# Kernel optimization log

Hardware: AMD Instinct MI355X
Metric: run time of the kernel (lower is better)

The kernel has to match this reference:

```python
import jax, jax.numpy as jnp
import numpy as np

NPOINT = 1024
RADIUS = 0.5
NSAMPLE = 32
BN_EPS = 1e-5


def square_distance(src, dst):
    # src: (B,S,3), dst: (B,N,3) -> (B,S,N)
    return (jnp.sum(src ** 2, -1, keepdims=True)
            + jnp.swapaxes(jnp.sum(dst ** 2, -1, keepdims=True), -2, -1)
            - 2.0 * jnp.einsum('bsc,bnc->bsn', src, dst))


def farthest_point_sample(xyz, npoint):
    # xyz: (B,N,3) -> (B,npoint) int32. Deterministic start at index 0.
    B, N, _ = xyz.shape

    def step(carry, _):
        distance, farthest = carry
        centroid = jnp.take_along_axis(xyz, farthest[:, None, None], axis=1)  # (B,1,3)
        d = jnp.sum((xyz - centroid) ** 2, axis=-1)                           # (B,N)
        distance = jnp.minimum(distance, d)
        nxt = jnp.argmax(distance, axis=-1).astype(jnp.int32)
        return (distance, nxt), farthest

    init = (jnp.full((B, N), 1e10, dtype=xyz.dtype), jnp.zeros((B,), jnp.int32))
    _, cents = jax.lax.scan(step, init, None, length=npoint)  # (npoint,B)
    return cents.T


def ball_query(radius, nsample, xyz, new_xyz):
    # -> (B,S,nsample) int32 indices into N; empty slots padded with first hit.
    B, N, _ = xyz.shape
    dist = square_distance(new_xyz, xyz)                       # (B,S,N)
    base = jnp.arange(N, dtype=jnp.int32)[None, None, :]
    idx = jnp.where(dist <= radius ** 2, base, N)
    idx = jnp.sort(idx, axis=-1)[:, :, :nsample]
    first = idx[:, :, :1]
    return jnp.where(idx == N, first, idx)


def index_points(points, idx):
    # points: (B,N,C), idx: (B,...) -> (B,...,C)
    return jax.vmap(lambda p, i: p[i])(points, idx)


def _forward(xyz, features, params):
    # indices are data-dependent but non-differentiable selections
    xyz_c = jax.lax.stop_gradient(xyz)
    fps_idx = farthest_point_sample(xyz_c, NPOINT)             # (B,S)
    group_idx = ball_query(RADIUS, NSAMPLE, xyz_c, index_points(xyz_c, fps_idx))

    new_xyz = index_points(xyz, fps_idx)                       # (B,S,3)
    grouped_xyz = index_points(xyz, group_idx) - new_xyz[:, :, None, :]  # (B,S,K,3)
    grouped = jnp.concatenate([grouped_xyz, index_points(features, group_idx)], -1)  # (B,S,K,Cin)

    for (w, b, g, be) in params:
        # 1x1 Conv2d == per-point linear; BatchNorm2d in training mode:
        # stats over all but channel axis (here axes 0,1,2 of (B,S,K,C)).
        h = jnp.einsum('bskc,dc->bskd', grouped, w) + b
        mean = jnp.mean(h, axis=(0, 1, 2))
        var = jnp.var(h, axis=(0, 1, 2))
        h = (h - mean) * jax.lax.rsqrt(var + BN_EPS) * g + be
        grouped = jax.nn.gelu(h, approximate=False)

    new_features = jnp.max(grouped, axis=2)                    # (B,S,D)
    return new_xyz, new_features


def setup_inputs() -> dict:
    key = jax.random.key(0)
    ks = jax.random.split(key, 16)
    B, N, C = 16, 4096, 64
    inp = {
        'xyz': jax.random.normal(ks[0], (B, N, 3), jnp.float32),
        'features': jax.random.normal(ks[1], (B, N, C), jnp.float32),
    }
    chans = [67, 64, 64, 128]
    for i in range(3):
        cin, cout = chans[i], chans[i + 1]
        inp[f'w{i}'] = jax.random.normal(ks[2 + 4 * i], (cout, cin), jnp.float32) * (1.0 / np.sqrt(cin))
        inp[f'b{i}'] = jnp.zeros((cout,), jnp.float32)
        inp[f'g{i}'] = jnp.ones((cout,), jnp.float32)
        inp[f'be{i}'] = jnp.zeros((cout,), jnp.float32)
    return inp


def reference(xyz, features, w0, b0, g0, be0, w1, b1, g1, be1, w2, b2, g2, be2):
    params = [(w0, b0, g0, be0), (w1, b1, g1, be1), (w2, b2, g2, be2)]
    return _forward(xyz, features, params)
```

## Files before the change

### kernel.cpp

```cpp
#include <hip/hip_runtime.h>

typedef unsigned int uint;
typedef unsigned short ushort;
typedef unsigned long long ull;

#define NB 16
#define NN 4096
#define NS 1024
#define NK 32
#define CIN0 67
#define NPTS (NB*NS*NK)
#define BN_EPS 1e-5f
#define INV_NPTS (1.0f/524288.0f)

#define W0T_OFF 0
#define W1T_OFF 4288
#define W2T_OFF 8384
#define WT_TOTAL 16576

#define FPS_T 256
#define PPT (NN / FPS_T)

#define KMAX_STEP(K, CTRL) do { \
    uint _lo = (uint)(K), _hi = (uint)((K) >> 32); \
    uint _nlo = (uint)__builtin_amdgcn_update_dpp(0, (int)_lo, (CTRL), 0xF, 0xF, true); \
    uint _nhi = (uint)__builtin_amdgcn_update_dpp(0, (int)_hi, (CTRL), 0xF, 0xF, true); \
    ull _nk = ((ull)_nhi << 32) | _nlo; \
    if (_nk > (K)) (K) = _nk; \
  } while (0)

__device__ __forceinline__ void fps_block_merge(
    const uint2* sk, const float4* sc,
    float& cx, float& cy, float& cz, int& fi)
{
  uint4 e01 = *(const uint4*)&sk[0];
  uint4 e23 = *(const uint4*)&sk[2];
  ull k0 = ((ull)e01.y << 32) | e01.x;
  ull k1 = ((ull)e01.w << 32) | e01.z;
  ull k2 = ((ull)e23.y << 32) | e23.x;
  ull k3 = ((ull)e23.w << 32) | e23.z;
  float4 c0 = sc[0], c1 = sc[1], c2 = sc[2], c3 = sc[3];
  ull b = k0; float4 C = c0;
  if (k1 > b) { b = k1; C = c1; }
  if (k2 > b) { b = k2; C = c2; }
  if (k3 > b) { b = k3; C = c3; }
  cx = C.x; cy = C.y; cz = C.z;
  fi = (int)(~(uint)b);
}

__global__ __launch_bounds__(FPS_T) void fps_kernel(
    const float* __restrict__ xyz, float* __restrict__ centers,
    float* __restrict__ out_newxyz)
{
#pragma clang fp contract(off)
  __shared__ float4 sxyz[NN];
  __shared__ int sfar[NS];
  __shared__ __align__(16) uint2  sk[2][FPS_T/64];
  __shared__ __align__(16) float4 sc[2][FPS_T/64];
  const int b = blockIdx.x;
  const int tid = threadIdx.x;
  const int lane = tid & 63;
  const int wv = tid >> 6;
  const float* xb = xyz + (size_t)b * NN * 3;
  for (int i = tid; i < NN; i += FPS_T)
    sxyz[i] = make_float4(xb[i*3+0], xb[i*3+1], xb[i*3+2], 0.f);
  __syncthreads();
  float px[PPT], py[PPT], pz[PPT], dist[PPT];
  const int base = tid * PPT;
#pragma unroll
  for (int j = 0; j < PPT; ++j) {
    float4 P = sxyz[base+j];
    px[j] = P.x; py[j] = P.y; pz[j] = P.z;
    dist[j] = 1e10f;
  }
  float4 C0 = sxyz[0];
  float cx = C0.x, cy = C0.y, cz = C0.z;
  if (tid == 0) sfar[0] = 0;

  for (int it = 1; it < NS; ++it) {
#pragma unroll
    for (int j = 0; j < PPT; ++j) {
      float dx = px[j]-cx, dy = py[j]-cy, dz = pz[j]-cz;
      float d = (dx*dx + dy*dy) + dz*dz;
      float dd = dist[j];
      dist[j] = d < dd ? d : dd;
    }
    float v8[8]; int i8[8];
#pragma unroll
    for (int j = 0; j < 8; ++j) {
      bool t = dist[2*j+1] > dist[2*j];
      v8[j] = t ? dist[2*j+1] : dist[2*j];
      i8[j] = base + (t ? 2*j+1 : 2*j);
    }
    float v4[4]; int i4[4];
#pragma unroll
    for (int j = 0; j < 4; ++j) {
      bool t = v8[2*j+1] > v8[2*j];
      v4[j] = t ? v8[2*j+1] : v8[2*j];
      i4[j] = t ? i8[2*j+1] : i8[2*j];
    }
    float v2[2]; int i2[2];
#pragma unroll
    for (int j = 0; j < 2; ++j) {
      bool t = v4[2*j+1] > v4[2*j];
      v2[j] = t ? v4[2*j+1] : v4[2*j];
      i2[j] = t ? i4[2*j+1] : i4[2*j];
    }
    bool t0 = v2[1] > v2[0];
    float bv = t0 ? v2[1] : v2[0];
    int   bi = t0 ? i2[1] : i2[0];
    ull key = ((ull)__float_as_uint(bv) << 32) | (uint)(~bi);
    KMAX_STEP(key, 0x121);
    KMAX_STEP(key, 0x122);
    KMAX_STEP(key, 0x124);
    KMAX_STEP(key, 0x128);
    KMAX_STEP(key, 0x142);
    KMAX_STEP(key, 0x143);
    const int pb = it & 1;
    if (lane == 63) {
      int iw = (int)(~(uint)key);
      float4 CW = sxyz[iw];
      sk[pb][wv] = make_uint2((uint)key, (uint)(key >> 32));
      sc[pb][wv] = CW;
    }
    __syncthreads();
    int fi;
    fps_block_merge(sk[pb], sc[pb], cx, cy, cz, fi);
    if (tid == 0) sfar[it] = fi;
  }
  __syncthreads();
  for (int s = tid; s < NS; s += FPS_T) {
    int f = sfar[s];
    float4 C = sxyz[f];
    size_t o = ((size_t)b * NS + s) * 3;
    centers[o] = C.x; centers[o+1] = C.y; centers[o+2] = C.z;
    out_newxyz[o] = C.x; out_newxyz[o+1] = C.y; out_newxyz[o+2] = C.z;
  }
}

#define BPAD(i) ((i) + ((i)>>6))
__global__ __launch_bounds__(256,2) void ball_kernel(
    const float* __restrict__ xyz, const float* __restrict__ centers,
    int* __restrict__ group_idx)
{
#pragma clang fp contract(off)
  __shared__ float sx[4160], sy[4160], sz[4160], sq[4160];
  const int bid = blockIdx.x;
  const int b = bid >> 6;
  const int c0 = (bid & 63) << 4;
  const int tid = threadIdx.x;
  const int lane = tid & 63;
  const int wave = tid >> 6;
  const float* xb = xyz + (size_t)b * NN * 3;
  for (int i = tid; i < NN; i += 256) {
    float x = xb[i*3+0], y = xb[i*3+1], z = xb[i*3+2];
    int a = BPAD(i);
    sx[a] = x; sy[a] = y; sz[a] = z;
    sq[a] = (x*x + y*y) + z*z;
  }
  __syncthreads();
  const int a0 = lane * 65;
#pragma unroll 1
  for (int r = 0; r < 4; ++r) {
    const int s = c0 + wave*4 + r;
    const size_t co = ((size_t)b * NS + s) * 3;
    const float cx = centers[co], cy = centers[co+1], cz = centers[co+2];
    const float csq = (cx*cx + cy*cy) + cz*cz;
    unsigned long long mask = 0ull;
#pragma unroll 8
    for (int j = 0; j < 64; ++j) {
      const float dot = (cx*sx[a0+j] + cy*sy[a0+j]) + cz*sz[a0+j];
      const float dist = (csq + sq[a0+j]) - 2.0f*dot;
      mask |= ((unsigned long long)(dist <= 0.25f)) << j;
    }
    int cnt = __popcll(mask);
    int inc = cnt;
#pragma unroll
    for (int m = 1; m < 64; m <<= 1) {
      int o = __shfl_up(inc, m);
      if (lane >= m) inc += o;
    }
    const int pre = inc - cnt;
    const int total = __shfl(inc, 63);
    unsigned long long bal = __ballot(cnt > 0);
    int fl = __ffsll(bal) - 1;
    int myfirst = cnt ? (lane << 6) + __ffsll(mask) - 1 : 0;
    int firstG = __shfl(myfirst, fl);
    int* out = group_idx + ((size_t)b * NS + s) * NK;
    if (pre < NK && cnt) {
      int k = pre;
      unsigned long long m2 = mask;
      while (m2 && k < NK) {
        int j = __ffsll(m2) - 1;
        out[k++] = (lane << 6) + j;
        m2 &= m2 - 1;
      }
    }
    if (total < NK) {
      for (int q2 = total + lane; q2 < NK; q2 += 64) out[q2] = firstG;
    }
  }
}

__global__ __launch_bounds__(256) void prep_kernel(
    const float* __restrict__ w0, const float* __restrict__ w1,
    const float* __restrict__ w2, float* __restrict__ wT)
{
  int i = blockIdx.x*256 + threadIdx.x;
  if (i < 4288) {
    int c = i >> 6, d = i & 63;
    wT[i] = w0[d*CIN0 + c];
  } else if (i < 8384) {
    int j = i - 4288; int c = j >> 6, d = j & 63;
    wT[i] = w1[d*64 + c];
  } else if (i < WT_TOTAL) {
    int j = i - 8384; int c = j >> 7, d = j & 127;
    wT[i] = w2[d*64 + c];
  }
}

__device__ __forceinline__ float gelu_f(float x) {
  float z = fabsf(x) * 0.70710678118654752f;
  float t = __builtin_amdgcn_rcpf(fmaf(0.3275911f, z, 1.0f));
  float p = t * fmaf(t, fmaf(t, fmaf(t, fmaf(t, 1.061405429f, -1.453152027f),
                                     1.421413741f), -0.284496736f), 0.254829592f);
  float ex = __expf(-z*z);
  float er = fmaf(-p, ex, 1.0f);
  float se = __uint_as_float(__float_as_uint(er) | (__float_as_uint(x) & 0x80000000u));
  return 0.5f * x * (1.0f + se);
}
__device__ __forceinline__ float bf_lo(uint u) { return __uint_as_float(u << 16); }
__device__ __forceinline__ float bf_hi(uint u) { return __uint_as_float(u & 0xffff0000u); }
__device__ __forceinline__ uint bfpack(float a, float b) {
  uint ua = __float_as_uint(a), ub = __float_as_uint(b);
  ua = (ua + 0x7fffu + ((ua >> 16) & 1u)) >> 16;
  ub = (ub + 0x7fffu + ((ub >> 16) & 1u)) >> 16;
  return (ua & 0xffffu) | (ub << 16);
}

__device__ __forceinline__ void fmac64(float (&acc)[64], const float* wrow, float xc) {
  const float4* wp = (const float4*)wrow;
#pragma unroll
  for (int i = 0; i < 16; ++i) {
    float4 w = wp[i];
    acc[i*4+0] = fmaf(xc, w.x, acc[i*4+0]);
    acc[i*4+1] = fmaf(xc, w.y, acc[i*4+1]);
    acc[i*4+2] = fmaf(xc, w.z, acc[i*4+2]);
    acc[i*4+3] = fmaf(xc, w.w, acc[i*4+3]);
  }
}
__device__ __forceinline__ void fmac128(float (&acc)[128], const float* wrow, float xc) {
  const float4* wp = (const float4*)wrow;
#pragma unroll
  for (int i = 0; i < 32; ++i) {
    float4 w = wp[i];
    acc[i*4+0] = fmaf(xc, w.x, acc[i*4+0]);
    acc[i*4+1] = fmaf(xc, w.y, acc[i*4+1]);
    acc[i*4+2] = fmaf(xc, w.z, acc[i*4+2]);
    acc[i*4+3] = fmaf(xc, w.w, acc[i*4+3]);
  }
}

__device__ __forceinline__ void layer0(
    const float* __restrict__ xyz, const float* __restrict__ feat,
    const float* __restrict__ centers, const int* __restrict__ gidx,
    const float* wptr, const float* b0v, int p, float (&acc)[64])
{
  const int b = p >> 15;
  const int s = (p & 32767) >> 5;
  const int gi = gidx[p];
#pragma unroll
  for (int d = 0; d < 64; ++d) acc[d] = b0v[d];
  const float* cp = centers + ((size_t)(b*NS + s))*3;
  const float* pp = xyz + ((size_t)(b*NN) + gi)*3;
  const float4* fr = (const float4*)(feat + ((size_t)(b*NN) + gi)*64);
  float4 f = fr[0];
  fmac64(acc, wptr + 0*64, pp[0]-cp[0]);
  fmac64(acc, wptr + 1*64, pp[1]-cp[1]);
  fmac64(acc, wptr + 2*64, pp[2]-cp[2]);
#pragma unroll 1
  for (int q = 0; q < 16; ++q) {
    const int nq = (q < 15) ? q + 1 : 15;
    float4 fn = fr[nq];
    fmac64(acc, wptr + (3+q*4)*64, f.x);
    fmac64(acc, wptr + (4+q*4)*64, f.y);
    fmac64(acc, wptr + (5+q*4)*64, f.z);
    fmac64(acc, wptr + (6+q*4)*64, f.w);
    f = fn;
  }
}

__device__ __forceinline__ void block_colsum64(const float (&v)[64], float* sbuf,
    float* bsum, float* bssq, int cbase)
{
  const int tid = threadIdx.x;
#pragma unroll
  for (int cc = 0; cc < 4; ++cc) {
    __syncthreads();
#pragma unroll
    for (int j = 0; j < 16; ++j) sbuf[tid*17 + j] = v[cc*16 + j];
    __syncthreads();
    const int c = tid & 15, seg = tid >> 4;
    float s = 0.f, q = 0.f;
#pragma unroll
    for (int i = 0; i < 16; ++i) {
      float x = sbuf[(seg*16 + i)*17 + c];
      s += x; q += x*x;
    }
    __syncthreads();
    sbuf[tid*2] = s; sbuf[tid*2+1] = q;
    __syncthreads();
    if (tid < 16) {
      float ss = 0.f, qq = 0.f;
#pragma unroll
      for (int sg = 0; sg < 16; ++sg) {
        ss += sbuf[(sg*16 + tid)*2];
        qq += sbuf[(sg*16 + tid)*2 + 1];
      }
      bsum[cbase + cc*16 + tid] += ss;
      bssq[cbase + cc*16 + tid] += qq;
    }
  }
  __syncthreads();
}

__global__ __launch_bounds__(256,3) void p0_kernel(
    const float* __restrict__ xyz, const float* __restrict__ feat,
    const float* __restrict__ centers, const int* __restrict__ gidx,
    const float* __restrict__ wT, const float* __restrict__ b0,
    ushort* __restrict__ X, float* __restrict__ stat0)
{
  __shared__ float sbuf[4352];
  __shared__ float bsum[64], bssq[64], b0s[64];
  const int tid = threadIdx.x;
  if (tid < 64) { bsum[tid] = 0.f; bssq[tid] = 0.f; b0s[tid] = b0[tid]; }
  __syncthreads();
  const int p = blockIdx.x*256 + tid;
  float acc[64];
  layer0(xyz, feat, centers, gidx, wT + W0T_OFF, b0s, p, acc);
  uint4* xr = (uint4*)(X + (size_t)p*64);
#pragma unroll
  for (int q = 0; q < 8; ++q) {
    uint4 pk;
    pk.x = bfpack(acc[q*8+0], acc[q*8+1]);
    pk.y = bfpack(acc[q*8+2], acc[q*8+3]);
    pk.z = bfpack(acc[q*8+4], acc[q*8+5]);
    pk.w = bfpack(acc[q*8+6], acc[q*8+7]);
    xr[q] = pk;
  }
  block_colsum64(acc, sbuf, bsum, bssq, 0);
  if (tid < 64) {
    atomicAdd(&stat0[tid], bsum[tid]);
    atomicAdd(&stat0[64+tid], bssq[tid]);
  }
}

__global__ __launch_bounds__(256,3) void p1_kernel(
    ushort* X, const float* __restrict__ wT,
    const float* __restrict__ stat0, const float* __restrict__ g0,
    const float* __restrict__ be0, const float* __restrict__ b1,
    float* __restrict__ stat1)
{
  __shared__ float sbuf[4352];
  __shared__ float bsum[64], bssq[64];
  __shared__ float sc[64], sh[64], b1s[64];
  const float* __restrict__ w1g = wT + W1T_OFF;
  const int tid = threadIdx.x;
  if (tid < 64) {
    float m0 = stat0[tid]*INV_NPTS;
    float v0 = stat0[64+tid]*INV_NPTS - m0*m0;
    float s0 = (1.0f/sqrtf(v0 + BN_EPS)) * g0[tid];
    sc[tid] = s0; sh[tid] = be0[tid] - m0*s0;
    b1s[tid] = b1[tid];
    bsum[tid] = 0.f; bssq[tid] = 0.f;
  }
  __syncthreads();
  const int p = blockIdx.x*256 + tid;
  uint4* xr = (uint4*)(X + (size_t)p*64);
  float acc[64];
#pragma unroll
  for (int d = 0; d < 64; ++d) acc[d] = b1s[d];
  uint4 v = xr[0];
#pragma unroll 1
  for (int ch = 0; ch < 8; ++ch) {
    const int nc = (ch < 7) ? ch + 1 : 7;
    uint4 vn = xr[nc];
    const int c = ch*8;
    float x0 = gelu_f(fmaf(bf_lo(v.x), sc[c+0], sh[c+0]));
    float x1 = gelu_f(fmaf(bf_hi(v.x), sc[c+1], sh[c+1]));
    float x2 = gelu_f(fmaf(bf_lo(v.y), sc[c+2], sh[c+2]));
    float x3 = gelu_f(fmaf(bf_hi(v.y), sc[c+3], sh[c+3]));
    float x4 = gelu_f(fmaf(bf_lo(v.z), sc[c+4], sh[c+4]));
    float x5 = gelu_f(fmaf(bf_hi(v.z), sc[c+5], sh[c+5]));
    float x6 = gelu_f(fmaf(bf_lo(v.w), sc[c+6], sh[c+6]));
    float x7 = gelu_f(fmaf(bf_hi(v.w), sc[c+7], sh[c+7]));
    fmac64(acc, w1g + (c+0)*64, x0);
    fmac64(acc, w1g + (c+1)*64, x1);
    fmac64(acc, w1g + (c+2)*64, x2);
    fmac64(acc, w1g + (c+3)*64, x3);
    fmac64(acc, w1g + (c+4)*64, x4);
    fmac64(acc, w1g + (c+5)*64, x5);
    fmac64(acc, w1g + (c+6)*64, x6);
    fmac64(acc, w1g + (c+7)*64, x7);
    v = vn;
  }
#pragma unroll
  for (int q = 0; q < 8; ++q) {
    uint4 pk;
    pk.x = bfpack(acc[q*8+0], acc[q*8+1]);
    pk.y = bfpack(acc[q*8+2], acc[q*8+3]);
    pk.z = bfpack(acc[q*8+4], acc[q*8+5]);
    pk.w = bfpack(acc[q*8+6], acc[q*8+7]);
    xr[q] = pk;
  }
  block_colsum64(acc, sbuf, bsum, bssq, 0);
  if (tid < 64) {
    atomicAdd(&stat1[tid], bsum[tid]);
    atomicAdd(&stat1[64+tid], bssq[tid]);
  }
}

template<bool STORE_H2>
__global__ __launch_bounds__(256,2) void p2_kernel(
    ushort* X, ushort* __restrict__ H2, const float* __restrict__ wT,
    const float* __restrict__ stat1, const float* __restrict__ g1,
    const float* __restrict__ be1, const float* __restrict__ b2,
    float* __restrict__ stat2)
{
  __shared__ float sbuf[4352];
  __shared__ float bsum[128], bssq[128];
  __shared__ float sc[64], sh[64], b2s[128];
  const float* __restrict__ w2g = wT + W2T_OFF;
  const int tid = threadIdx.x;
  if (tid < 64) {
    float m1 = stat1[tid]*INV_NPTS;
    float v1 = stat1[64+tid]*INV_NPTS - m1*m1;
    float s1 = (1.0f/sqrtf(v1 + BN_EPS)) * g1[tid];
    sc[tid] = s1; sh[tid] = be1[tid] - m1*s1;
  }
  if (tid < 128) { b2s[tid] = b2[tid]; bsum[tid] = 0.f; bssq[tid] = 0.f; }
  __syncthreads();
  const int p = blockIdx.x*256 + tid;
  uint4* xr = (uint4*)(X + (size_t)p*64);
  float acc[128];
#pragma unroll
  for (int d = 0; d < 128; ++d) acc[d] = b2s[d];
  uint4 v = xr[0];
#pragma unroll 1
  for (int ch = 0; ch < 8; ++ch) {
    const int nc = (ch < 7) ? ch + 1 : 7;
    uint4 vn = xr[nc];
    const int c = ch*8;
    float x0 = gelu_f(fmaf(bf_lo(v.x), sc[c+0], sh[c+0]));
    float x1 = gelu_f(fmaf(bf_hi(v.x), sc[c+1], sh[c+1]));
    float x2 = gelu_f(fmaf(bf_lo(v.y), sc[c+2], sh[c+2]));
    float x3 = gelu_f(fmaf(bf_hi(v.y), sc[c+3], sh[c+3]));
    float x4 = gelu_f(fmaf(bf_lo(v.z), sc[c+4], sh[c+4]));
    float x5 = gelu_f(fmaf(bf_hi(v.z), sc[c+5], sh[c+5]));
    float x6 = gelu_f(fmaf(bf_lo(v.w), sc[c+6], sh[c+6]));
    float x7 = gelu_f(fmaf(bf_hi(v.w), sc[c+7], sh[c+7]));
    if (!STORE_H2) {
      uint4 pk;
      pk.x = bfpack(x0, x1); pk.y = bfpack(x2, x3);
      pk.z = bfpack(x4, x5); pk.w = bfpack(x6, x7);
      xr[ch] = pk;
    }
    fmac128(acc, w2g + (c+0)*128, x0);
    fmac128(acc, w2g + (c+1)*128, x1);
    fmac128(acc, w2g + (c+2)*128, x2);
    fmac128(acc, w2g + (c+3)*128, x3);
    fmac128(acc, w2g + (c+4)*128, x4);
    fmac128(acc, w2g + (c+5)*128, x5);
    fmac128(acc, w2g + (c+6)*128, x6);
    fmac128(acc, w2g + (c+7)*128, x7);
    v = vn;
  }
  if (STORE_H2) {
    uint4* hr = (uint4*)(H2 + (size_t)p*128);
#pragma unroll
    for (int q = 0; q < 16; ++q) {
      uint4 pk;
      pk.x = bfpack(acc[q*8+0], acc[q*8+1]);
      pk.y = bfpack(acc[q*8+2], acc[q*8+3]);
      pk.z = bfpack(acc[q*8+4], acc[q*8+5]);
      pk.w = bfpack(acc[q*8+6], acc[q*8+7]);
      hr[q] = pk;
    }
  }
#pragma unroll
  for (int half = 0; half < 2; ++half) {
    float tmp[64];
#pragma unroll
    for (int d = 0; d < 64; ++d) tmp[d] = acc[half*64 + d];
    block_colsum64(tmp, sbuf, bsum, bssq, half*64);
  }
  if (tid < 128) {
    atomicAdd(&stat2[tid], bsum[tid]);
    atomicAdd(&stat2[128+tid], bssq[tid]);
  }
}

__global__ __launch_bounds__(128) void fbig_kernel(
    const ushort* __restrict__ H2, const float* __restrict__ stat2,
    const float* __restrict__ g2, const float* __restrict__ be2,
    float* __restrict__ out_feat)
{
  const int d = threadIdx.x;
  const int bs = blockIdx.x;
  const float mean = stat2[d] * INV_NPTS;
  const float var  = stat2[128+d] * INV_NPTS - mean*mean;
  const float scale = (1.0f/sqrtf(var + BN_EPS)) * g2[d];
  const float shift = be2[d] - mean*scale;
  const ushort* rp = H2 + (size_t)bs*NK*128 + d;
  float m = -3.4e38f;
#pragma unroll 4
  for (int k = 0; k < NK; ++k) {
    float t = __uint_as_float(((uint)rp[k*128]) << 16);
    m = fmaxf(m, gelu_f(fmaf(t, scale, shift)));
  }
  out_feat[(size_t)bs*128 + d] = m;
}

__global__ __launch_bounds__(256,2) void fsmall_kernel(
    const ushort* __restrict__ X, const float* __restrict__ wT,
    const float* __restrict__ b2, const float* __restrict__ stat2,
    const float* __restrict__ g2, const float* __restrict__ be2,
    float* __restrict__ out_feat)
{
  __shared__ float b2s[128], sc2[128], sh2[128];
  const float* __restrict__ w2g = wT + W2T_OFF;
  const int tid = threadIdx.x;
  if (tid < 128) {
    b2s[tid] = b2[tid];
    float m2 = stat2[tid]*INV_NPTS;
    float v2 = stat2[128+tid]*INV_NPTS - m2*m2;
    float s2 = (1.0f/sqrtf(v2 + BN_EPS)) * g2[tid];
    sc2[tid] = s2; sh2[tid] = be2[tid] - m2*s2;
  }
  __syncthreads();
  const int p = blockIdx.x*256 + tid;
  const int bs = p >> 5;
  const uint4* xr = (const uint4*)(X + (size_t)p*64);
  float acc[128];
#pragma unroll
  for (int d = 0; d < 128; ++d) acc[d] = b2s[d];
  uint4 v = xr[0];
#pragma unroll 1
  for (int ch = 0; ch < 8; ++ch) {
    const int nc = (ch < 7) ? ch + 1 : 7;
    uint4 vn = xr[nc];
    const int c = ch*8;
    fmac128(acc, w2g + (c+0)*128, bf_lo(v.x));
    fmac128(acc, w2g + (c+1)*128, bf_hi(v.x));
    fmac128(acc, w2g + (c+2)*128, bf_lo(v.y));
    fmac128(acc, w2g + (c+3)*128, bf_hi(v.y));
    fmac128(acc, w2g + (c+4)*128, bf_lo(v.z));
    fmac128(acc, w2g + (c+5)*128, bf_hi(v.z));
    fmac128(acc, w2g + (c+6)*128, bf_lo(v.w));
    fmac128(acc, w2g + (c+7)*128, bf_hi(v.w));
    v = vn;
  }
#pragma unroll
  for (int d = 0; d < 128; ++d) {
    float y = gelu_f(fmaf(acc[d], sc2[d], sh2[d]));
#pragma unroll
    for (int m = 1; m < 32; m <<= 1) y = fmaxf(y, __shfl_xor(y, m));
    acc[d] = y;
  }
  if ((tid & 31) == 0) {
    float4* op = (float4*)(out_feat + (size_t)bs*128);
#pragma unroll
    for (int i = 0; i < 32; ++i)
      op[i] = make_float4(acc[i*4], acc[i*4+1], acc[i*4+2], acc[i*4+3]);
  }
}

__device__ __forceinline__ void chain_to_x2(
    const float* __restrict__ xyz, const float* __restrict__ feat,
    const float* __restrict__ centers, const int* __restrict__ gidx,
    const float* wsh, float* sbuf, const float* prm, int p, float (&x2)[64])
{
  float acc0[64];
  layer0(xyz, feat, centers, gidx, wsh, prm, p, acc0);
#pragma unroll
  for (int c = 0; c < 64; ++c) acc0[c] = gelu_f(fmaf(acc0[c], prm[64+c], prm[128+c]));
#pragma unroll
  for (int d = 0; d < 64; ++d) x2[d] = prm[192+d];
  float* xrow = sbuf + threadIdx.x*17;
#pragma unroll
  for (int cc = 0; cc < 4; ++cc) {
#pragma unroll
    for (int j = 0; j < 16; ++j) xrow[j] = acc0[cc*16 + j];
#pragma unroll 1
    for (int cj = 0; cj < 16; ++cj)
      fmac64(x2, wsh + W1T_OFF + (cc*16+cj)*64, xrow[cj]);
  }
#pragma unroll
  for (int c = 0; c < 64; ++c) x2[c] = gelu_f(fmaf(x2[c], prm[256+c], prm[320+c]));
}

__global__ __launch_bounds__(256,2) void s0_kernel(
    const float* __restrict__ xyz, const float* __restrict__ feat,
    const float* __restrict__ centers, const int* __restrict__ gidx,
    const float* __restrict__ wT, const float* __restrict__ b0,
    float* __restrict__ stat0)
{
  __shared__ float wsh[4288];
  __shared__ float sbuf[4352];
  __shared__ float bsum[64], bssq[64], b0s[64];
  const int tid = threadIdx.x;
  for (int i = tid; i < 1072; i += 256) ((float4*)wsh)[i] = ((const float4*)wT)[i];
  if (tid < 64) { bsum[tid] = 0.f; bssq[tid] = 0.f; b0s[tid] = b0[tid]; }
  __syncthreads();
  const int p = blockIdx.x*256 + tid;
  float acc[64];
  layer0(xyz, feat, centers, gidx, wsh, b0s, p, acc);
  block_colsum64(acc, sbuf, bsum, bssq, 0);
  if (tid < 64) {
    atomicAdd(&stat0[tid], bsum[tid]);
    atomicAdd(&stat0[64+tid], bssq[tid]);
  }
}

__global__ __launch_bounds__(256,2) void s1_kernel(
    const float* __restrict__ xyz, const float* __restrict__ feat,
    const float* __restrict__ centers, const int* __restrict__ gidx,
    const float* __restrict__ wT, const float* __restrict__ stat0,
    const float* __restrict__ g0, const float* __restrict__ be0,
    const float* __restrict__ b0, const float* __restrict__ b1,
    float* __restrict__ stat1)
{
  __shared__ float wsh[8384];
  __shared__ float sbuf[4352];
  __shared__ float bsum[64], bssq[64];
  __shared__ float prm[256];
  const int tid = threadIdx.x;
  for (int i = tid; i < 2096; i += 256) ((float4*)wsh)[i] = ((const float4*)wT)[i];
  if (tid < 64) {
    float m0 = stat0[tid]*INV_NPTS;
    float v0 = stat0[64+tid]*INV_NPTS - m0*m0;
    float sc0 = (1.0f/sqrtf(v0 + BN_EPS)) * g0[tid];
    prm[tid] = b0[tid]; prm[64+tid] = sc0; prm[128+tid] = be0[tid] - m0*sc0;
    prm[192+tid] = b1[tid];
    bsum[tid] = 0.f; bssq[tid] = 0.f;
  }
  __syncthreads();
  const int p = blockIdx.x*256 + tid;
  float acc0[64];
  layer0(xyz, feat, centers, gidx, wsh, prm, p, acc0);
#pragma unroll
  for (int c = 0; c < 64; ++c) acc0[c] = gelu_f(fmaf(acc0[c], prm[64+c], prm[128+c]));
  float acc1[64];
#pragma unroll
  for (int d = 0; d < 64; ++d) acc1[d] = prm[192+d];
  float* xrow = sbuf + tid*17;
#pragma unroll
  for (int cc = 0; cc < 4; ++cc) {
#pragma unroll
    for (int j = 0; j < 16; ++j) xrow[j] = acc0[cc*16 + j];
#pragma unroll 1
    for (int cj = 0; cj < 16; ++cj)
      fmac64(acc1, wsh + W1T_OFF + (cc*16+cj)*64, xrow[cj]);
  }
  block_colsum64(acc1, sbuf, bsum, bssq, 0);
  if (tid < 64) {
    atomicAdd(&stat1[tid], bsum[tid]);
    atomicAdd(&stat1[64+tid], bssq[tid]);
  }
}

__global__ __launch_bounds__(256,2) void s2_kernel(
    const float* __restrict__ xyz, const float* __restrict__ feat,
    const float* __restrict__ centers, const int* __restrict__ gidx,
    const float* __restrict__ wT,
    const float* __restrict__ stat0, const float* __restrict__ g0,
    const float* __restrict__ be0, const float* __restrict__ b0,
    const float* __restrict__ b1, const float* __restrict__ stat1,
    const float* __restrict__ g1, const float* __restrict__ be1,
    const float* __restrict__ b2, float* __restrict__ stat2)
{
  __shared__ float wsh[8384];
  __shared__ float sbuf[4352];
  __shared__ float bsum[128], bssq[128];
  __shared__ float prm[512];
  const int tid = threadIdx.x;
  for (int i = tid; i < 2096; i += 256) ((float4*)wsh)[i] = ((const float4*)wT)[i];
  if (tid < 64) {
    float m0 = stat0[tid]*INV_NPTS;
    float v0 = stat0[64+tid]*INV_NPTS - m0*m0;
    float sc0 = (1.0f/sqrtf(v0 + BN_EPS)) * g0[tid];
    prm[tid] = b0[tid]; prm[64+tid] = sc0; prm[128+tid] = be0[tid] - m0*sc0;
    float m1 = stat1[tid]*INV_NPTS;
    float v1 = stat1[64+tid]*INV_NPTS - m1*m1;
    float sc1 = (1.0f/sqrtf(v1 + BN_EPS)) * g1[tid];
    prm[192+tid] = b1[tid]; prm[256+tid] = sc1; prm[320+tid] = be1[tid] - m1*sc1;
  }
  if (tid < 128) { prm[384+tid] = b2[tid]; bsum[tid] = 0.f; bssq[tid] = 0.f; }
  __syncthreads();
  const int p = blockIdx.x*256 + tid;
  float x2[64];
  chain_to_x2(xyz, feat, centers, gidx, wsh, sbuf, prm, p, x2);
  __syncthreads();
  for (int i = tid; i < 2048; i += 256)
    ((float4*)wsh)[i] = ((const float4*)(wT + W2T_OFF))[i];
  __syncthreads();
  float* xrow = sbuf + tid*17;
#pragma unroll 1
  for (int half = 0; half < 2; ++half) {
    float a2[64];
#pragma unroll
    for (int d = 0; d < 64; ++d) a2[d] = prm[384 + half*64 + d];
#pragma unroll
    for (int cc = 0; cc < 4; ++cc) {
#pragma unroll
      for (int j = 0; j < 16; ++j) xrow[j] = x2[cc*16 + j];
#pragma unroll 1
      for (int cj = 0; cj < 16; ++cj)
        fmac64(a2, wsh + (cc*16+cj)*128 + half*64, xrow[cj]);
    }
    block_colsum64(a2, sbuf, bsum, bssq, half*64);
  }
  if (tid < 128) {
    atomicAdd(&stat2[tid], bsum[tid]);
    atomicAdd(&stat2[128+tid], bssq[tid]);
  }
}

__global__ __launch_bounds__(256,2) void fin_kernel(
    const float* __restrict__ xyz, const float* __restrict__ feat,
    const float* __restrict__ centers, const int* __restrict__ gidx,
    const float* __restrict__ wT,
    const float* __restrict__ stat0, const float* __restrict__ g0,
    const float* __restrict__ be0, const float* __restrict__ b0,
    const float* __restrict__ b1, const float* __restrict__ stat1,
    const float* __restrict__ g1, const float* __restrict__ be1,
    const float* __restrict__ b2, const float* __restrict__ stat2,
    const float* __restrict__ g2, const float* __restrict__ be2,
    float* __restrict__ out_feat)
{
  __shared__ float wsh[8384];
  __shared__ float sbuf[4352];
  __shared__ float prm[768];
  const int tid = threadIdx.x;
  for (int i = tid; i < 2096; i += 256) ((float4*)wsh)[i] = ((const float4*)wT)[i];
  if (tid < 64) {
    float m0 = stat0[tid]*INV_NPTS;
    float v0 = stat0[64+tid]*INV_NPTS - m0*m0;
    float sc0 = (1.0f/sqrtf(v0 + BN_EPS)) * g0[tid];
    prm[tid] = b0[tid]; prm[64+tid] = sc0; prm[128+tid] = be0[tid] - m0*sc0;
    float m1 = stat1[tid]*INV_NPTS;
    float v1 = stat1[64+tid]*INV_NPTS - m1*m1;
    float sc1 = (1.0f/sqrtf(v1 + BN_EPS)) * g1[tid];
    prm[192+tid] = b1[tid]; prm[256+tid] = sc1; prm[320+tid] = be1[tid] - m1*sc1;
  }
  if (tid < 128) {
    prm[384+tid] = b2[tid];
    float m2 = stat2[tid]*INV_NPTS;
    float v2 = stat2[128+tid]*INV_NPTS - m2*m2;
    float sc2 = (1.0f/sqrtf(v2 + BN_EPS)) * g2[tid];
    prm[512+tid] = sc2; prm[640+tid] = be2[tid] - m2*sc2;
  }
  __syncthreads();
  const int p = blockIdx.x*256 + tid;
  const int b = p >> 15;
  const int s = (p & 32767) >> 5;
  float x2[64];
  chain_to_x2(xyz, feat, centers, gidx, wsh, sbuf, prm, p, x2);
  __syncthreads();
  for (int i = tid; i < 2048; i += 256)
    ((float4*)wsh)[i] = ((const float4*)(wT + W2T_OFF))[i];
  __syncthreads();
  float* xrow = sbuf + tid*17;
#pragma unroll 1
  for (int half = 0; half < 2; ++half) {
    float a2[64];
#pragma unroll
    for (int d = 0; d < 64; ++d) a2[d] = prm[384 + half*64 + d];
#pragma unroll
    for (int cc = 0; cc < 4; ++cc) {
#pragma unroll
      for (int j = 0; j < 16; ++j) xrow[j] = x2[cc*16 + j];
#pragma unroll 1
      for (int cj = 0; cj < 16; ++cj)
        fmac64(a2, wsh + (cc*16+cj)*128 + half*64, xrow[cj]);
    }
#pragma unroll
    for (int d = 0; d < 64; ++d) {
      float y = gelu_f(fmaf(a2[d], prm[512 + half*64 + d], prm[640 + half*64 + d]));
#pragma unroll
      for (int m = 1; m < 32; m <<= 1) y = fmaxf(y, __shfl_xor(y, m));
      a2[d] = y;
    }
    if ((tid & 31) == 0) {
      float4* op = (float4*)(out_feat + ((size_t)(b*NS + s))*128 + half*64);
#pragma unroll
      for (int i = 0; i < 16; ++i)
        op[i] = make_float4(a2[i*4], a2[i*4+1], a2[i*4+2], a2[i*4+3]);
    }
  }
}

extern "C" void kernel_launch(void* const* d_in, const int* in_sizes, int n_in,
                              void* d_out, int out_size, void* d_ws, size_t ws_size,
                              hipStream_t stream) {
  (void)in_sizes; (void)n_in; (void)out_size;
  const float* xyz      = (const float*)d_in[0];
  const float* features = (const float*)d_in[1];
  const float* w0  = (const float*)d_in[2];
  const float* b0  = (const float*)d_in[3];
  const float* g0  = (const float*)d_in[4];
  const float* be0 = (const float*)d_in[5];
  const float* w1  = (const float*)d_in[6];
  const float* b1  = (const float*)d_in[7];
  const float* g1  = (const float*)d_in[8];
  const float* be1 = (const float*)d_in[9];
  const float* w2  = (const float*)d_in[10];
  const float* b2  = (const float*)d_in[11];
  const float* g2  = (const float*)d_in[12];
  const float* be2 = (const float*)d_in[13];

  float* out = (float*)d_out;
  float* out_newxyz = out;
  float* out_feat   = out + NB*NS*3;

  char* ws = (char*)d_ws;
  size_t off = 0;
  float* centers   = (float*)(ws + off); off += (size_t)NB*NS*3*4;
  int*   group_idx = (int*)(ws + off);   off += (size_t)NPTS*4;
  float* stats     = (float*)(ws + off); off += 512*4;
  off = (off + 255) & ~(size_t)255;
  float* wT        = (float*)(ws + off); off += (size_t)WT_TOTAL*4;
  off = (off + 255) & ~(size_t)255;
  const size_t base_end = off;
  const size_t X_bytes  = (size_t)NPTS*64*2;
  const size_t H2_bytes = (size_t)NPTS*128*2;
  ushort* X  = (ushort*)(ws + base_end);
  ushort* H2 = (ushort*)(ws + base_end + X_bytes);

  const bool tier_big   = ws_size >= base_end + X_bytes + H2_bytes;
  const bool tier_small = !tier_big && ws_size >= base_end + X_bytes;
  if (ws_size < base_end) return;

  float* stat0 = stats;
  float* stat1 = stats + 128;
  float* stat2 = stats + 256;

  (void)hipMemsetAsync(stats, 0, 2048, stream);
  prep_kernel<<<65, 256, 0, stream>>>(w0, w1, w2, wT);
  fps_kernel<<<NB, FPS_T, 0, stream>>>(xyz, centers, out_newxyz);
  ball_kernel<<<NB*64, 256, 0, stream>>>(xyz, centers, group_idx);

  if (tier_big || tier_small) {
    p0_kernel<<<NPTS/256, 256, 0, stream>>>(xyz, features, centers, group_idx,
                                            wT, b0, X, stat0);
    p1_kernel<<<NPTS/256, 256, 0, stream>>>(X, wT, stat0, g0, be0, b1, stat1);
    if (tier_big) {
      p2_kernel<true><<<NPTS/256, 256, 0, stream>>>(X, H2, wT, stat1, g1, be1, b2, stat2);
      fbig_kernel<<<NB*NS, 128, 0, stream>>>(H2, stat2, g2, be2, out_feat);
    } else {
      p2_kernel<false><<<NPTS/256, 256, 0, stream>>>(X, H2, wT, stat1, g1, be1, b2, stat2);
      fsmall_kernel<<<NPTS/256, 256, 0, stream>>>(X, wT, b2, stat2, g2, be2, out_feat);
    }
  } else {
    s0_kernel<<<NPTS/256, 256, 0, stream>>>(xyz, features, centers, group_idx, wT, b0, stat0);
    s1_kernel<<<NPTS/256, 256, 0, stream>>>(xyz, features, centers, group_idx, wT,
                                            stat0, g0, be0, b0, b1, stat1);
    s2_kernel<<<NPTS/256, 256, 0, stream>>>(xyz, features, centers, group_idx, wT,
                                            stat0, g0, be0, b0, b1, stat1, g1, be1, b2, stat2);
    fin_kernel<<<NPTS/256, 256, 0, stream>>>(xyz, features, centers, group_idx, wT,
                                             stat0, g0, be0, b0, b1, stat1, g1, be1, b2,
                                             stat2, g2, be2, out_feat);
  }
}
```

Before: 1.366 ms.

## Precompute per-point feature projection, move BN stats to separate passes, split FPS argmax

```diff
diff --git a/kernel.cpp b/kernel.cpp
--- a/kernel.cpp
+++ b/kernel.cpp
@@ -10,6 +10,7 @@
 #define NK 32
 #define CIN0 67
 #define NPTS (NB*NS*NK)
+#define NROWS (NB*NN)
 #define BN_EPS 1e-5f
 #define INV_NPTS (1.0f/524288.0f)
 
@@ -21,12 +22,13 @@
 #define FPS_T 256
 #define PPT (NN / FPS_T)
 
-#define KMAX_STEP(K, CTRL) do { \
-    uint _lo = (uint)(K), _hi = (uint)((K) >> 32); \
-    uint _nlo = (uint)__builtin_amdgcn_update_dpp(0, (int)_lo, (CTRL), 0xF, 0xF, true); \
-    uint _nhi = (uint)__builtin_amdgcn_update_dpp(0, (int)_hi, (CTRL), 0xF, 0xF, true); \
-    ull _nk = ((ull)_nhi << 32) | _nlo; \
-    if (_nk > (K)) (K) = _nk; \
+#define DPP_FMAX(M, CTRL) do { \
+    int _o = __builtin_amdgcn_update_dpp(0, __float_as_int(M), (CTRL), 0xF, 0xF, true); \
+    (M) = fmaxf((M), __int_as_float(_o)); \
+  } while (0)
+#define DPP_IMIN(C, CTRL) do { \
+    int _o = __builtin_amdgcn_update_dpp(0, (C), (CTRL), 0xF, 0xF, true); \
+    (C) = (C) < _o ? (C) : _o; \
   } while (0)
 
 __device__ __forceinline__ void fps_block_merge(
@@ -109,17 +111,18 @@
     bool t0 = v2[1] > v2[0];
     float bv = t0 ? v2[1] : v2[0];
     int   bi = t0 ? i2[1] : i2[0];
-    ull key = ((ull)__float_as_uint(bv) << 32) | (uint)(~bi);
-    KMAX_STEP(key, 0x121);
-    KMAX_STEP(key, 0x122);
-    KMAX_STEP(key, 0x124);
-    KMAX_STEP(key, 0x128);
-    KMAX_STEP(key, 0x142);
-    KMAX_STEP(key, 0x143);
+    float m = bv;
+    DPP_FMAX(m, 0x121); DPP_FMAX(m, 0x122); DPP_FMAX(m, 0x124);
+    DPP_FMAX(m, 0x128); DPP_FMAX(m, 0x142); DPP_FMAX(m, 0x143);
+    float maxv = __int_as_float(__builtin_amdgcn_readlane(__float_as_int(m), 63));
+    int cand = (bv == maxv) ? bi : 0x7fffffff;
+    DPP_IMIN(cand, 0x121); DPP_IMIN(cand, 0x122); DPP_IMIN(cand, 0x124);
+    DPP_IMIN(cand, 0x128); DPP_IMIN(cand, 0x142); DPP_IMIN(cand, 0x143);
     const int pb = it & 1;
     if (lane == 63) {
-      int iw = (int)(~(uint)key);
+      int iw = cand;
       float4 CW = sxyz[iw];
+      ull key = ((ull)__float_as_uint(maxv) << 32) | (uint)(~iw);
       sk[pb][wv] = make_uint2((uint)key, (uint)(key >> 32));
       sc[pb][wv] = CW;
     }
@@ -324,20 +327,114 @@
   __syncthreads();
 }
 
+__global__ __launch_bounds__(256,3) void f0_kernel(
+    const float* __restrict__ feat, const float* __restrict__ wT,
+    const float* __restrict__ b0, float* __restrict__ F0)
+{
+  const int r = blockIdx.x*256 + threadIdx.x;
+  const float* wf = wT + W0T_OFF + 3*64;
+  float acc[64];
+#pragma unroll
+  for (int d = 0; d < 64; ++d) acc[d] = b0[d];
+  const float4* fr = (const float4*)(feat + (size_t)r*64);
+  float4 f = fr[0];
+#pragma unroll 1
+  for (int q = 0; q < 16; ++q) {
+    const int nq = (q < 15) ? q + 1 : 15;
+    float4 fn = fr[nq];
+    fmac64(acc, wf + (q*4+0)*64, f.x);
+    fmac64(acc, wf + (q*4+1)*64, f.y);
+    fmac64(acc, wf + (q*4+2)*64, f.z);
+    fmac64(acc, wf + (q*4+3)*64, f.w);
+    f = fn;
+  }
+  float4* orow = (float4*)(F0 + (size_t)r*64);
+#pragma unroll
+  for (int q = 0; q < 16; ++q)
+    orow[q] = make_float4(acc[q*4], acc[q*4+1], acc[q*4+2], acc[q*4+3]);
+}
+
+__global__ __launch_bounds__(256) void xstat_kernel(
+    const ushort* __restrict__ X, float* __restrict__ stat)
+{
+  __shared__ float red[256][4];
+  const int tid = threadIdx.x;
+  const uint* xp = (const uint*)X;
+  size_t i = (size_t)blockIdx.x*256 + tid;
+  float s0=0,q0=0,s1=0,q1=0;
+  for (; i < (size_t)NPTS*32; i += 65536) {
+    uint v = xp[i];
+    float a = bf_lo(v), b = bf_hi(v);
+    s0 += a; q0 += a*a; s1 += b; q1 += b*b;
+  }
+  red[tid][0]=s0; red[tid][1]=q0; red[tid][2]=s1; red[tid][3]=q1;
+  __syncthreads();
+  if (tid < 32) {
+    for (int j = tid+32; j < 256; j += 32) {
+      s0+=red[j][0]; q0+=red[j][1]; s1+=red[j][2]; q1+=red[j][3];
+    }
+    atomicAdd(&stat[2*tid+0], s0); atomicAdd(&stat[64+2*tid+0], q0);
+    atomicAdd(&stat[2*tid+1], s1); atomicAdd(&stat[64+2*tid+1], q1);
+  }
+}
+
+__global__ __launch_bounds__(256) void h2stat_kernel(
+    const ushort* __restrict__ H2, float* __restrict__ stat)
+{
+  __shared__ float red[256][4];
+  const int tid = threadIdx.x;
+  const uint* hp = (const uint*)H2;
+  size_t i = (size_t)blockIdx.x*256 + tid;
+  float s0=0,q0=0,s1=0,q1=0;
+  for (; i < (size_t)NPTS*64; i += 65536) {
+    uint v = hp[i];
+    float a = bf_lo(v), b = bf_hi(v);
+    s0 += a; q0 += a*a; s1 += b; q1 += b*b;
+  }
+  red[tid][0]=s0; red[tid][1]=q0; red[tid][2]=s1; red[tid][3]=q1;
+  __syncthreads();
+  if (tid < 64) {
+    for (int j = tid+64; j < 256; j += 64) {
+      s0+=red[j][0]; q0+=red[j][1]; s1+=red[j][2]; q1+=red[j][3];
+    }
+    atomicAdd(&stat[2*tid+0], s0); atomicAdd(&stat[128+2*tid+0], q0);
+    atomicAdd(&stat[2*tid+1], s1); atomicAdd(&stat[128+2*tid+1], q1);
+  }
+}
+
+template<bool WITH_F0>
 __global__ __launch_bounds__(256,3) void p0_kernel(
     const float* __restrict__ xyz, const float* __restrict__ feat,
     const float* __restrict__ centers, const int* __restrict__ gidx,
     const float* __restrict__ wT, const float* __restrict__ b0,
-    ushort* __restrict__ X, float* __restrict__ stat0)
-{
-  __shared__ float sbuf[4352];
-  __shared__ float bsum[64], bssq[64], b0s[64];
-  const int tid = threadIdx.x;
-  if (tid < 64) { bsum[tid] = 0.f; bssq[tid] = 0.f; b0s[tid] = b0[tid]; }
-  __syncthreads();
+    const float* __restrict__ F0, ushort* __restrict__ X)
+{
+  __shared__ float b0s[64];
+  const int tid = threadIdx.x;
+  if constexpr (!WITH_F0) {
+    if (tid < 64) b0s[tid] = b0[tid];
+    __syncthreads();
+  }
   const int p = blockIdx.x*256 + tid;
   float acc[64];
-  layer0(xyz, feat, centers, gidx, wT + W0T_OFF, b0s, p, acc);
+  if constexpr (WITH_F0) {
+    const int b = p >> 15;
+    const int s = (p & 32767) >> 5;
+    const int gi = gidx[p];
+    const float4* f0r = (const float4*)(F0 + ((size_t)(b*NN) + gi)*64);
+#pragma unroll
+    for (int q = 0; q < 16; ++q) {
+      float4 v = f0r[q];
+      acc[q*4+0] = v.x; acc[q*4+1] = v.y; acc[q*4+2] = v.z; acc[q*4+3] = v.w;
+    }
+    const float* cp = centers + ((size_t)(b*NS + s))*3;
+    const float* pp = xyz + ((size_t)(b*NN) + gi)*3;
+    fmac64(acc, wT + W0T_OFF + 0*64, pp[0]-cp[0]);
+    fmac64(acc, wT + W0T_OFF + 1*64, pp[1]-cp[1]);
+    fmac64(acc, wT + W0T_OFF + 2*64, pp[2]-cp[2]);
+  } else {
+    layer0(xyz, feat, centers, gidx, wT + W0T_OFF, b0s, p, acc);
+  }
   uint4* xr = (uint4*)(X + (size_t)p*64);
 #pragma unroll
   for (int q = 0; q < 8; ++q) {
@@ -348,21 +445,13 @@
     pk.w = bfpack(acc[q*8+6], acc[q*8+7]);
     xr[q] = pk;
   }
-  block_colsum64(acc, sbuf, bsum, bssq, 0);
-  if (tid < 64) {
-    atomicAdd(&stat0[tid], bsum[tid]);
-    atomicAdd(&stat0[64+tid], bssq[tid]);
-  }
 }
 
 __global__ __launch_bounds__(256,3) void p1_kernel(
     ushort* X, const float* __restrict__ wT,
     const float* __restrict__ stat0, const float* __restrict__ g0,
-    const float* __restrict__ be0, const float* __restrict__ b1,
-    float* __restrict__ stat1)
-{
-  __shared__ float sbuf[4352];
-  __shared__ float bsum[64], bssq[64];
+    const float* __restrict__ be0, const float* __restrict__ b1)
+{
   __shared__ float sc[64], sh[64], b1s[64];
   const float* __restrict__ w1g = wT + W1T_OFF;
   const int tid = threadIdx.x;
@@ -372,7 +461,6 @@
     float s0 = (1.0f/sqrtf(v0 + BN_EPS)) * g0[tid];
     sc[tid] = s0; sh[tid] = be0[tid] - m0*s0;
     b1s[tid] = b1[tid];
-    bsum[tid] = 0.f; bssq[tid] = 0.f;
   }
   __syncthreads();
   const int p = blockIdx.x*256 + tid;
@@ -413,11 +501,6 @@
     pk.w = bfpack(acc[q*8+6], acc[q*8+7]);
     xr[q] = pk;
   }
-  block_colsum64(acc, sbuf, bsum, bssq, 0);
-  if (tid < 64) {
-    atomicAdd(&stat1[tid], bsum[tid]);
-    atomicAdd(&stat1[64+tid], bssq[tid]);
-  }
 }
 
 template<bool STORE_H2>
@@ -486,17 +569,18 @@
       pk.w = bfpack(acc[q*8+6], acc[q*8+7]);
       hr[q] = pk;
     }
-  }
-#pragma unroll
-  for (int half = 0; half < 2; ++half) {
-    float tmp[64];
-#pragma unroll
-    for (int d = 0; d < 64; ++d) tmp[d] = acc[half*64 + d];
-    block_colsum64(tmp, sbuf, bsum, bssq, half*64);
-  }
-  if (tid < 128) {
-    atomicAdd(&stat2[tid], bsum[tid]);
-    atomicAdd(&stat2[128+tid], bssq[tid]);
+  } else {
+#pragma unroll
+    for (int half = 0; half < 2; ++half) {
+      float tmp[64];
+#pragma unroll
+      for (int d = 0; d < 64; ++d) tmp[d] = acc[half*64 + d];
+      block_colsum64(tmp, sbuf, bsum, bssq, half*64);
+    }
+    if (tid < 128) {
+      atomicAdd(&stat2[tid], bsum[tid]);
+      atomicAdd(&stat2[128+tid], bssq[tid]);
+    }
   }
 }
 
@@ -834,12 +918,17 @@
   const size_t base_end = off;
   const size_t X_bytes  = (size_t)NPTS*64*2;
   const size_t H2_bytes = (size_t)NPTS*128*2;
+  const size_t F0_bytes = (size_t)NROWS*64*4;
   ushort* X  = (ushort*)(ws + base_end);
   ushort* H2 = (ushort*)(ws + base_end + X_bytes);
 
   const bool tier_big   = ws_size >= base_end + X_bytes + H2_bytes;
   const bool tier_small = !tier_big && ws_size >= base_end + X_bytes;
   if (ws_size < base_end) return;
+  const size_t f0_off = tier_big ? base_end + X_bytes + H2_bytes
+                                 : base_end + X_bytes;
+  const bool use_f0 = (tier_big || tier_small) && (ws_size >= f0_off + F0_bytes);
+  float* F0 = (float*)(ws + f0_off);
 
   float* stat0 = stats;
   float* stat1 = stats + 128;
@@ -847,15 +936,24 @@
 
   (void)hipMemsetAsync(stats, 0, 2048, stream);
   prep_kernel<<<65, 256, 0, stream>>>(w0, w1, w2, wT);
+  if (use_f0)
+    f0_kernel<<<NROWS/256, 256, 0, stream>>>(features, wT, b0, F0);
   fps_kernel<<<NB, FPS_T, 0, stream>>>(xyz, centers, out_newxyz);
   ball_kernel<<<NB*64, 256, 0, stream>>>(xyz, centers, group_idx);
 
   if (tier_big || tier_small) {
-    p0_kernel<<<NPTS/256, 256, 0, stream>>>(xyz, features, centers, group_idx,
-                                            wT, b0, X, stat0);
-    p1_kernel<<<NPTS/256, 256, 0, stream>>>(X, wT, stat0, g0, be0, b1, stat1);
+    if (use_f0)
+      p0_kernel<true><<<NPTS/256, 256, 0, stream>>>(xyz, features, centers, group_idx,
+                                                    wT, b0, F0, X);
+    else
+      p0_kernel<false><<<NPTS/256, 256, 0, stream>>>(xyz, features, centers, group_idx,
+                                                     wT, b0, F0, X);
+    xstat_kernel<<<256, 256, 0, stream>>>(X, stat0);
+    p1_kernel<<<NPTS/256, 256, 0, stream>>>(X, wT, stat0, g0, be0, b1);
+    xstat_kernel<<<256, 256, 0, stream>>>(X, stat1);
     if (tier_big) {
       p2_kernel<true><<<NPTS/256, 256, 0, stream>>>(X, H2, wT, stat1, g1, be1, b2, stat2);
+      h2stat_kernel<<<256, 256, 0, stream>>>(H2, stat2);
       fbig_kernel<<<NB*NS, 128, 0, stream>>>(H2, stat2, g2, be2, out_feat);
     } else {
       p2_kernel<false><<<NPTS/256, 256, 0, stream>>>(X, H2, wT, stat1, g1, be1, b2, stat2);
```

Result: slower. 2.016 ms (+47.6%).
